# Kernel optimization log

Hardware: AMD Instinct MI355X
Metric: run time of the kernel (lower is better)

## Reference

```python
import jax, jax.numpy as jnp
import numpy as np

NEG_SLOPE = 0.2

def setup_inputs() -> dict:
    key = jax.random.key(0)
    k1, k2, k3, k4 = jax.random.split(key, 4)
    N, K, C_IN, C_OUT = 8192, 4, 512, 512
    inputs = jax.random.normal(k1, (N, C_IN), dtype=jnp.float32)
    adj_set = jax.random.uniform(k2, (K, N, N), dtype=jnp.float32)
    att = jax.random.uniform(k3, (K,), dtype=jnp.float32)
    # xavier_uniform for w
    limit = float(np.sqrt(6.0 / (C_IN + C_OUT)))
    w = jax.random.uniform(k4, (C_IN, C_OUT), minval=-limit, maxval=limit, dtype=jnp.float32)
    b = jnp.zeros((C_OUT,), dtype=jnp.float32)
    return {"inputs": inputs, "adj_set": adj_set, "att": att, "w": w, "b": b}

def reference(inputs, adj_set, att, w, b):
    # support: [N, C_out]
    support = inputs @ w + b
    # residual=True path: outputs = sum_i att[i] * (adj_i @ support)
    #                             = (sum_i att[i] * adj_i) @ support
    combined_adj = jnp.einsum('k,knm->nm', att, adj_set)  # [N, N]
    outputs = combined_adj @ support                       # [N, C_out]
    # LeakyReLU(negative_slope=0.2)
    return jnp.where(outputs >= 0, outputs, NEG_SLOPE * outputs)
```

## Files before the change

### kernel.cpp

```cpp
#include <hip/hip_runtime.h>

#define LP 40

typedef __attribute__((ext_vector_type(8))) short short8;
typedef __attribute__((ext_vector_type(4))) short short4t;
typedef __attribute__((ext_vector_type(4))) float f32x4;

__device__ __forceinline__ short f2bf(float f) {
  unsigned u = __builtin_bit_cast(unsigned, f);
  u += 0x7FFFu + ((u >> 16) & 1u);
  return (short)(u >> 16);
}

__device__ __forceinline__ float lrelu(float v) { return v >= 0.f ? v : 0.2f * v; }

__global__ __launch_bounds__(256) void k_wt(const float* __restrict__ w,
                                            short* __restrict__ wt) {
  __shared__ float t[64][65];
  int c0 = (blockIdx.x & 7) * 64;
  int n0 = (blockIdx.x >> 3) * 64;
  int r  = threadIdx.x >> 4;
  int q4 = (threadIdx.x & 15) * 4;
  for (int i = 0; i < 4; i++) {
    int c = r + i * 16;
    f32x4 v = *(const f32x4*)(w + (size_t)(c0 + c) * 512 + (n0 + q4));
    t[c][q4 + 0] = v[0]; t[c][q4 + 1] = v[1]; t[c][q4 + 2] = v[2]; t[c][q4 + 3] = v[3];
  }
  __syncthreads();
  for (int i = 0; i < 4; i++) {
    int n = r + i * 16;
    short4t o;
    for (int j = 0; j < 4; j++) o[j] = f2bf(t[q4 + j][n]);
    *(short4t*)(wt + (size_t)(n0 + n) * 512 + (c0 + q4)) = o;
  }
}

__global__ __launch_bounds__(512, 2) void k_support(const float* __restrict__ inp,
                                                    const short* __restrict__ wt,
                                                    const float* __restrict__ bias,
                                                    short* __restrict__ sup) {
  __shared__ __align__(16) short As[512 * LP];
  __shared__ __align__(16) short Bs[64 * LP];
  const int tid = threadIdx.x;
  const int m0 = blockIdx.x * 64;
  const int wave = tid >> 6, lane = tid & 63;
  const int wn = wave >> 1, wm = wave & 1;
  const int lr = lane & 15, lk = lane >> 4;
  const int bm = tid >> 3, bk = (tid & 7) * 4;
  f32x4 acc[8][2] = {};
  short8 ar[4]; f32x4 br;
  auto loadA = [&](int s) {
    const short* p = wt + (size_t)tid * 512 + s * 32;
    ar[0] = *(const short8*)(p);      ar[1] = *(const short8*)(p + 8);
    ar[2] = *(const short8*)(p + 16); ar[3] = *(const short8*)(p + 24);
  };
  auto loadB = [&](int s) {
    br = *(const f32x4*)(inp + (size_t)(m0 + bm) * 512 + s * 32 + bk);
  };
  loadA(0); loadB(0);
  for (int s = 0; s < 16; s++) {
    short* ad = As + tid * LP;
    *(short8*)(ad) = ar[0]; *(short8*)(ad + 8) = ar[1];
    *(short8*)(ad + 16) = ar[2]; *(short8*)(ad + 24) = ar[3];
    short4t bo;
    for (int j = 0; j < 4; j++) bo[j] = f2bf(br[j]);
    *(short4t*)(Bs + bm * LP + bk) = bo;
    __syncthreads();
    if (s + 1 < 16) { loadA(s + 1); loadB(s + 1); }
    short8 af[8], bfr[2];
    for (int nf = 0; nf < 8; nf++)
      af[nf] = *(const short8*)(As + (wn * 128 + nf * 16 + lr) * LP + lk * 8);
    for (int mf = 0; mf < 2; mf++)
      bfr[mf] = *(const short8*)(Bs + (wm * 32 + mf * 16 + lr) * LP + lk * 8);
    for (int nf = 0; nf < 8; nf++)
      for (int mf = 0; mf < 2; mf++)
        acc[nf][mf] = __builtin_amdgcn_mfma_f32_16x16x32_bf16(af[nf], bfr[mf], acc[nf][mf], 0, 0, 0);
    __syncthreads();
  }
  for (int nf = 0; nf < 8; nf++) {
    int nb = wn * 128 + nf * 16 + lk * 4;
    for (int mf = 0; mf < 2; mf++) {
      int m = m0 + wm * 32 + mf * 16 + lr;
      for (int j = 0; j < 4; j++) {
        int n = nb + j;
        sup[(size_t)n * 8192 + m] = f2bf(acc[nf][mf][j] + bias[n]);
      }
    }
  }
}

__global__ __launch_bounds__(512, 2) void k_main(const float* __restrict__ adj,
                                                 const float* __restrict__ att,
                                                 const short* __restrict__ sup,
                                                 float* __restrict__ part,
                                                 float* __restrict__ outp,
                                                 int ksplit) {
  __shared__ __align__(16) short Bs[2][128 * LP];
  const int tid = threadIdx.x;
  const int b = blockIdx.x;
  const int xpk = 8 / ksplit;
  const int xcd = b & 7;
  const int kc = xcd / xpk;
  const int m0 = ((b >> 3) * xpk + (xcd % xpk)) * 128;
  const int kchunk = 8192 / ksplit;
  const int nsteps = kchunk / 32;
  const int kbase = kc * kchunk;
  const float t0 = att[0], t1 = att[1], t2 = att[2], t3 = att[3];
  const int wave = tid >> 6, lane = tid & 63;
  const int lr = lane & 15, lk = lane >> 4;
  const int srow = tid >> 2, koff = (tid & 3) * 8;
  f32x4 acc[4][8] = {};
  const float* adjp = adj + (size_t)(m0 + srow) * 8192 + kbase + koff;
  const short* supp = sup + (size_t)(wave * 64 + lr) * 8192 + kbase + lk * 8;
  f32x4 br[8];
  auto loadAdj = [&](int s) {
    const float* q = adjp + (size_t)s * 32;
#pragma unroll
    for (int mt = 0; mt < 4; mt++) {
      br[mt * 2]     = __builtin_nontemporal_load((const f32x4*)(q + ((size_t)mt << 26)));
      br[mt * 2 + 1] = __builtin_nontemporal_load((const f32x4*)(q + ((size_t)mt << 26) + 4));
    }
  };
  loadAdj(0);
  int p = 0;
  for (int s = 0; s < nsteps; s++) {
    short8 af[4];
#pragma unroll
    for (int nf = 0; nf < 4; nf++)
      af[nf] = *(const short8*)(supp + (size_t)(nf * 16) * 8192 + s * 32);
    short8 bo;
#pragma unroll
    for (int k2 = 0; k2 < 8; k2++) {
      int h = k2 >> 2, j = k2 & 3;
      float c = t0 * br[h][j] + t1 * br[2 + h][j] + t2 * br[4 + h][j] + t3 * br[6 + h][j];
      bo[k2] = f2bf(c);
    }
    *(short8*)(Bs[p] + srow * LP + koff) = bo;
    __syncthreads();
    if (s + 1 < nsteps) loadAdj(s + 1);
    short8 bfr[8];
#pragma unroll
    for (int mf = 0; mf < 8; mf++)
      bfr[mf] = *(const short8*)(Bs[p] + (mf * 16 + lr) * LP + lk * 8);
#pragma unroll
    for (int nf = 0; nf < 4; nf++)
#pragma unroll
      for (int mf = 0; mf < 8; mf++)
        acc[nf][mf] = __builtin_amdgcn_mfma_f32_16x16x32_bf16(af[nf], bfr[mf], acc[nf][mf], 0, 0, 0);
    p ^= 1;
  }
#pragma unroll
  for (int nf = 0; nf < 4; nf++) {
    int n = wave * 64 + nf * 16 + lk * 4;
#pragma unroll
    for (int mf = 0; mf < 8; mf++) {
      int m = m0 + mf * 16 + lr;
      f32x4 v = acc[nf][mf];
      if (ksplit == 1) {
        for (int j = 0; j < 4; j++) v[j] = lrelu(v[j]);
        __builtin_nontemporal_store(v, (f32x4*)(outp + (size_t)m * 512 + n));
      } else {
        __builtin_nontemporal_store(v, (f32x4*)(part + ((size_t)kc << 22) + (size_t)m * 512 + n));
      }
    }
  }
}

__global__ __launch_bounds__(256) void k_reduce(const float* __restrict__ part,
                                                float* __restrict__ outp, int ksplit) {
  const size_t total = (size_t)8192 * 512 / 4;
  for (size_t i = (size_t)blockIdx.x * 256 + threadIdx.x; i < total;
       i += (size_t)gridDim.x * 256) {
    f32x4 a = __builtin_nontemporal_load((const f32x4*)(part + i * 4));
    for (int k = 1; k < ksplit; k++) {
      f32x4 bv = __builtin_nontemporal_load((const f32x4*)(part + ((size_t)k << 22) + i * 4));
      for (int j = 0; j < 4; j++) a[j] += bv[j];
    }
    f32x4 v;
    for (int j = 0; j < 4; j++) v[j] = lrelu(a[j]);
    __builtin_nontemporal_store(v, (f32x4*)(outp + i * 4));
  }
}

extern "C" void kernel_launch(void* const* d_in, const int* in_sizes, int n_in,
                              void* d_out, int out_size, void* d_ws, size_t ws_size,
                              hipStream_t stream) {
  const float* inputs = (const float*)d_in[0];
  const float* adj    = (const float*)d_in[1];
  const float* att    = (const float*)d_in[2];
  const float* w      = (const float*)d_in[3];
  const float* bias   = (const float*)d_in[4];
  float* outp = (float*)d_out;

  char* ws = (char*)d_ws;
  short* sup  = (short*)(ws);
  short* wt   = (short*)(ws + (8u << 20));
  float* part = (float*)(ws + (9u << 20));

  const size_t base = (9ull << 20), psz = (1ull << 24);
  int ksplit = 1;
  if (ws_size >= base + 4 * psz) ksplit = 4;
  else if (ws_size >= base + 2 * psz) ksplit = 2;

  k_wt<<<64, 256, 0, stream>>>(w, wt);
  k_support<<<128, 512, 0, stream>>>(inputs, wt, bias, sup);
  k_main<<<64 * ksplit, 512, 0, stream>>>(adj, att, sup, part, outp, ksplit);
  if (ksplit > 1) k_reduce<<<1024, 256, 0, stream>>>(part, outp, ksplit);
}
```

Measured before the change: 337.3 us.

## Stream adjacency one matrix at a time over 128-wide K tiles in k_main

The main kernel's K step grows from 32 to 128. The adjacency loads are restructured so each thread streams one of the four adjacency matrices at a time through a two-slot register buffer, accumulating the weighted sum while the next matrix's load is in flight. This cuts barrier count per K and gives longer contiguous per-row reads, but enlarges the LDS tile (padded stride 136) and register pressure, which may reduce occupancy.

```diff
diff --git a/kernel.cpp b/kernel.cpp
--- a/kernel.cpp
+++ b/kernel.cpp
@@ -1,6 +1,7 @@
 #include <hip/hip_runtime.h>
 
-#define LP 40
+#define LP  40
+#define LPS 136
 
 typedef __attribute__((ext_vector_type(8))) short short8;
 typedef __attribute__((ext_vector_type(4))) short short4t;
@@ -95,7 +96,7 @@
                                                  float* __restrict__ part,
                                                  float* __restrict__ outp,
                                                  int ksplit) {
-  __shared__ __align__(16) short Bs[2][128 * LP];
+  __shared__ __align__(16) short Bs[2][128 * LPS];
   const int tid = threadIdx.x;
   const int b = blockIdx.x;
   const int xpk = 8 / ksplit;
@@ -103,50 +104,62 @@
   const int kc = xcd / xpk;
   const int m0 = ((b >> 3) * xpk + (xcd % xpk)) * 128;
   const int kchunk = 8192 / ksplit;
-  const int nsteps = kchunk / 32;
+  const int nbig = kchunk / 128;
   const int kbase = kc * kchunk;
   const float t0 = att[0], t1 = att[1], t2 = att[2], t3 = att[3];
   const int wave = tid >> 6, lane = tid & 63;
   const int lr = lane & 15, lk = lane >> 4;
-  const int srow = tid >> 2, koff = (tid & 3) * 8;
+  const int r = tid >> 2, q = tid & 3;
   f32x4 acc[4][8] = {};
-  const float* adjp = adj + (size_t)(m0 + srow) * 8192 + kbase + koff;
+  const float* abase = adj + (size_t)(m0 + r) * 8192 + kbase + q * 4;
   const short* supp = sup + (size_t)(wave * 64 + lr) * 8192 + kbase + lk * 8;
-  f32x4 br[8];
-  auto loadAdj = [&](int s) {
-    const float* q = adjp + (size_t)s * 32;
-#pragma unroll
-    for (int mt = 0; mt < 4; mt++) {
-      br[mt * 2]     = __builtin_nontemporal_load((const f32x4*)(q + ((size_t)mt << 26)));
-      br[mt * 2 + 1] = __builtin_nontemporal_load((const f32x4*)(q + ((size_t)mt << 26) + 4));
-    }
+
+  f32x4 R[2][8];
+  auto loadMat = [&](int slot, int mat, int s) {
+    const float* p = abase + ((size_t)mat << 26) + s * 128;
+#pragma unroll
+    for (int j = 0; j < 8; j++)
+      R[slot][j] = __builtin_nontemporal_load((const f32x4*)(p + j * 16));
   };
-  loadAdj(0);
+  loadMat(0, 0, 0);
   int p = 0;
-  for (int s = 0; s < nsteps; s++) {
-    short8 af[4];
-#pragma unroll
-    for (int nf = 0; nf < 4; nf++)
-      af[nf] = *(const short8*)(supp + (size_t)(nf * 16) * 8192 + s * 32);
-    short8 bo;
-#pragma unroll
-    for (int k2 = 0; k2 < 8; k2++) {
-      int h = k2 >> 2, j = k2 & 3;
-      float c = t0 * br[h][j] + t1 * br[2 + h][j] + t2 * br[4 + h][j] + t3 * br[6 + h][j];
-      bo[k2] = f2bf(c);
-    }
-    *(short8*)(Bs[p] + srow * LP + koff) = bo;
+  for (int s = 0; s < nbig; s++) {
+    f32x4 par[8];
+    loadMat(1, 1, s);
+#pragma unroll
+    for (int j = 0; j < 8; j++) { f32x4 v = R[0][j]; for (int e = 0; e < 4; e++) par[j][e] = t0 * v[e]; }
+    loadMat(0, 2, s);
+#pragma unroll
+    for (int j = 0; j < 8; j++) { f32x4 v = R[1][j]; for (int e = 0; e < 4; e++) par[j][e] += t1 * v[e]; }
+    loadMat(1, 3, s);
+#pragma unroll
+    for (int j = 0; j < 8; j++) { f32x4 v = R[0][j]; for (int e = 0; e < 4; e++) par[j][e] += t2 * v[e]; }
+    if (s + 1 < nbig) loadMat(0, 0, s + 1);
+#pragma unroll
+    for (int j = 0; j < 8; j++) { f32x4 v = R[1][j]; for (int e = 0; e < 4; e++) par[j][e] += t3 * v[e]; }
+    short* brow = Bs[p] + r * LPS + q * 4;
+#pragma unroll
+    for (int j = 0; j < 8; j++) {
+      short4t o;
+      for (int e = 0; e < 4; e++) o[e] = f2bf(par[j][e]);
+      *(short4t*)(brow + j * 16) = o;
+    }
     __syncthreads();
-    if (s + 1 < nsteps) loadAdj(s + 1);
-    short8 bfr[8];
-#pragma unroll
-    for (int mf = 0; mf < 8; mf++)
-      bfr[mf] = *(const short8*)(Bs[p] + (mf * 16 + lr) * LP + lk * 8);
-#pragma unroll
-    for (int nf = 0; nf < 4; nf++)
+#pragma unroll
+    for (int sub = 0; sub < 4; sub++) {
+      short8 af[4], bfr[8];
+#pragma unroll
+      for (int nf = 0; nf < 4; nf++)
+        af[nf] = *(const short8*)(supp + (size_t)(nf * 16) * 8192 + s * 128 + sub * 32);
 #pragma unroll
       for (int mf = 0; mf < 8; mf++)
-        acc[nf][mf] = __builtin_amdgcn_mfma_f32_16x16x32_bf16(af[nf], bfr[mf], acc[nf][mf], 0, 0, 0);
+        bfr[mf] = *(const short8*)(Bs[p] + (mf * 16 + lr) * LPS + sub * 32 + lk * 8);
+#pragma unroll
+      for (int nf = 0; nf < 4; nf++)
+#pragma unroll
+        for (int mf = 0; mf < 8; mf++)
+          acc[nf][mf] = __builtin_amdgcn_mfma_f32_16x16x32_bf16(af[nf], bfr[mf], acc[nf][mf], 0, 0, 0);
+    }
     p ^= 1;
   }
 #pragma unroll
```

After: 356.4 us. +5.7%, slower.

## Deepen adjacency prefetch to three steps with smaller M tiles and ksplit 2

Applied to the files above, without the earlier changes.

Halves the k_main M tile from 128 to 64 rows so each thread loads one float4 per adjacency slice, and doubles the block count. Adjacency loads are now issued three k-steps ahead through a four-slot register ring in a manually unrolled loop, to keep more HBM requests in flight on this bandwidth-bound stream. The K split drops from 4 to 2, which shrinks the partial-sum buffer and the reduce traffic. In exchange, the support operand is re-read from memory by twice as many row tiles, and the register ring adds register pressure.

```diff
diff --git a/kernel.cpp b/kernel.cpp
--- a/kernel.cpp
+++ b/kernel.cpp
@@ -1,6 +1,7 @@
 #include <hip/hip_runtime.h>
 
-#define LP 40
+#define LP  40
+#define LPB 40
 
 typedef __attribute__((ext_vector_type(8))) short short8;
 typedef __attribute__((ext_vector_type(4))) short short4t;
@@ -89,71 +90,72 @@
   }
 }
 
+#define ISSUE(SL, S) {                                                          \
+    const float* p_ = abase + (size_t)(S) * 32;                                 \
+    R[SL][0] = __builtin_nontemporal_load((const f32x4*)(p_));                  \
+    R[SL][1] = __builtin_nontemporal_load((const f32x4*)(p_ + (1ull << 26)));   \
+    R[SL][2] = __builtin_nontemporal_load((const f32x4*)(p_ + (2ull << 26)));   \
+    R[SL][3] = __builtin_nontemporal_load((const f32x4*)(p_ + (3ull << 26)));   \
+  }
+
+#define STEP(U) {                                                               \
+    const int s_ = s0 + (U);                                                    \
+    if (s_ + 3 < nsteps) ISSUE(((U) + 3) & 3, s_ + 3);                          \
+    short8 af[4];                                                               \
+    _Pragma("unroll") for (int nf = 0; nf < 4; nf++)                            \
+      af[nf] = *(const short8*)(supp + (size_t)(nf * 16) * 8192 + (size_t)s_ * 32); \
+    f32x4 c;                                                                    \
+    _Pragma("unroll") for (int e = 0; e < 4; e++)                               \
+      c[e] = t0 * R[(U)][0][e] + t1 * R[(U)][1][e]                              \
+           + t2 * R[(U)][2][e] + t3 * R[(U)][3][e];                             \
+    short4t o;                                                                  \
+    _Pragma("unroll") for (int e = 0; e < 4; e++) o[e] = f2bf(c[e]);            \
+    *(short4t*)(Bs[(U) & 1] + r * LPB + q * 4) = o;                             \
+    __syncthreads();                                                            \
+    short8 bfr[4];                                                              \
+    _Pragma("unroll") for (int mf = 0; mf < 4; mf++)                            \
+      bfr[mf] = *(const short8*)(Bs[(U) & 1] + (mf * 16 + lr) * LPB + lk * 8);  \
+    _Pragma("unroll") for (int nf = 0; nf < 4; nf++)                            \
+      _Pragma("unroll") for (int mf = 0; mf < 4; mf++)                          \
+        acc[nf][mf] = __builtin_amdgcn_mfma_f32_16x16x32_bf16(af[nf], bfr[mf],  \
+                                                              acc[nf][mf], 0, 0, 0); \
+  }
+
 __global__ __launch_bounds__(512, 2) void k_main(const float* __restrict__ adj,
                                                  const float* __restrict__ att,
                                                  const short* __restrict__ sup,
                                                  float* __restrict__ part,
                                                  float* __restrict__ outp,
                                                  int ksplit) {
-  __shared__ __align__(16) short Bs[2][128 * LP];
+  __shared__ __align__(16) short Bs[2][64 * LPB];
   const int tid = threadIdx.x;
   const int b = blockIdx.x;
   const int xpk = 8 / ksplit;
   const int xcd = b & 7;
   const int kc = xcd / xpk;
-  const int m0 = ((b >> 3) * xpk + (xcd % xpk)) * 128;
+  const int m0 = ((b >> 3) * xpk + (xcd % xpk)) * 64;
   const int kchunk = 8192 / ksplit;
   const int nsteps = kchunk / 32;
   const int kbase = kc * kchunk;
   const float t0 = att[0], t1 = att[1], t2 = att[2], t3 = att[3];
   const int wave = tid >> 6, lane = tid & 63;
   const int lr = lane & 15, lk = lane >> 4;
-  const int srow = tid >> 2, koff = (tid & 3) * 8;
-  f32x4 acc[4][8] = {};
-  const float* adjp = adj + (size_t)(m0 + srow) * 8192 + kbase + koff;
+  const int r = tid >> 3, q = tid & 7;
+  f32x4 acc[4][4] = {};
+  const float* abase = adj + (size_t)(m0 + r) * 8192 + kbase + q * 4;
   const short* supp = sup + (size_t)(wave * 64 + lr) * 8192 + kbase + lk * 8;
-  f32x4 br[8];
-  auto loadAdj = [&](int s) {
-    const float* q = adjp + (size_t)s * 32;
-#pragma unroll
-    for (int mt = 0; mt < 4; mt++) {
-      br[mt * 2]     = __builtin_nontemporal_load((const f32x4*)(q + ((size_t)mt << 26)));
-      br[mt * 2 + 1] = __builtin_nontemporal_load((const f32x4*)(q + ((size_t)mt << 26) + 4));
-    }
-  };
-  loadAdj(0);
-  int p = 0;
-  for (int s = 0; s < nsteps; s++) {
-    short8 af[4];
-#pragma unroll
-    for (int nf = 0; nf < 4; nf++)
-      af[nf] = *(const short8*)(supp + (size_t)(nf * 16) * 8192 + s * 32);
-    short8 bo;
-#pragma unroll
-    for (int k2 = 0; k2 < 8; k2++) {
-      int h = k2 >> 2, j = k2 & 3;
-      float c = t0 * br[h][j] + t1 * br[2 + h][j] + t2 * br[4 + h][j] + t3 * br[6 + h][j];
-      bo[k2] = f2bf(c);
-    }
-    *(short8*)(Bs[p] + srow * LP + koff) = bo;
-    __syncthreads();
-    if (s + 1 < nsteps) loadAdj(s + 1);
-    short8 bfr[8];
-#pragma unroll
-    for (int mf = 0; mf < 8; mf++)
-      bfr[mf] = *(const short8*)(Bs[p] + (mf * 16 + lr) * LP + lk * 8);
-#pragma unroll
-    for (int nf = 0; nf < 4; nf++)
-#pragma unroll
-      for (int mf = 0; mf < 8; mf++)
-        acc[nf][mf] = __builtin_amdgcn_mfma_f32_16x16x32_bf16(af[nf], bfr[mf], acc[nf][mf], 0, 0, 0);
-    p ^= 1;
-  }
+  f32x4 R[4][4];
+
+  ISSUE(0, 0); ISSUE(1, 1); ISSUE(2, 2);
+  for (int s0 = 0; s0 < nsteps; s0 += 4) {
+    STEP(0) STEP(1) STEP(2) STEP(3)
+  }
+
 #pragma unroll
   for (int nf = 0; nf < 4; nf++) {
     int n = wave * 64 + nf * 16 + lk * 4;
 #pragma unroll
-    for (int mf = 0; mf < 8; mf++) {
+    for (int mf = 0; mf < 4; mf++) {
       int m = m0 + mf * 16 + lr;
       f32x4 v = acc[nf][mf];
       if (ksplit == 1) {
@@ -198,12 +200,10 @@
   float* part = (float*)(ws + (9u << 20));
 
   const size_t base = (9ull << 20), psz = (1ull << 24);
-  int ksplit = 1;
-  if (ws_size >= base + 4 * psz) ksplit = 4;
-  else if (ws_size >= base + 2 * psz) ksplit = 2;
+  int ksplit = (ws_size >= base + 2 * psz) ? 2 : 1;
 
   k_wt<<<64, 256, 0, stream>>>(w, wt);
   k_support<<<128, 512, 0, stream>>>(inputs, wt, bias, sup);
-  k_main<<<64 * ksplit, 512, 0, stream>>>(adj, att, sup, part, outp, ksplit);
+  k_main<<<128 * ksplit, 512, 0, stream>>>(adj, att, sup, part, outp, ksplit);
   if (ksplit > 1) k_reduce<<<1024, 256, 0, stream>>>(part, outp, ksplit);
 }
```

Result: faster. 317.7 us (-5.8%).

## Stream adjacency tiles into LDS via global_load_lds with 1024-thread blocks

Applied to the files above, without the earlier changes.

The main kernel now loads adjacency tiles straight from global memory into a double-buffered LDS staging area with global_load_lds, instead of through registers. It then combines the four attention-weighted matrices from LDS into bf16. The block grows to 1024 threads (16 waves) with a 2x8 wave tiling, which halves the per-wave accumulators, and synchronisation uses explicit waitcnt, sched_barrier and s_barrier. This is meant to raise the number of memory requests in flight and hide HBM latency on the bandwidth-bound adjacency stream. In exchange it uses about 136KB of LDS per block, and the hand-written waitcnt and wrap-around prefetch bring correctness and scheduling risk.

```diff
diff --git a/kernel.cpp b/kernel.cpp
--- a/kernel.cpp
+++ b/kernel.cpp
@@ -1,6 +1,7 @@
 #include <hip/hip_runtime.h>
 
-#define LP 40
+#define LP  40
+#define LPB 40
 
 typedef __attribute__((ext_vector_type(8))) short short8;
 typedef __attribute__((ext_vector_type(4))) short short4t;
@@ -89,13 +90,14 @@
   }
 }
 
-__global__ __launch_bounds__(512, 2) void k_main(const float* __restrict__ adj,
-                                                 const float* __restrict__ att,
-                                                 const short* __restrict__ sup,
-                                                 float* __restrict__ part,
-                                                 float* __restrict__ outp,
-                                                 int ksplit) {
-  __shared__ __align__(16) short Bs[2][128 * LP];
+__global__ __launch_bounds__(1024, 4) void k_main(const float* __restrict__ adj,
+                                                  const float* __restrict__ att,
+                                                  const short* __restrict__ sup,
+                                                  float* __restrict__ part,
+                                                  float* __restrict__ outp,
+                                                  int ksplit) {
+  __shared__ __align__(16) float rawA[2][4 * 128 * 32];
+  __shared__ __align__(16) short Bs[2][128 * LPB];
   const int tid = threadIdx.x;
   const int b = blockIdx.x;
   const int xpk = 8 / ksplit;
@@ -106,55 +108,81 @@
   const int nsteps = kchunk / 32;
   const int kbase = kc * kchunk;
   const float t0 = att[0], t1 = att[1], t2 = att[2], t3 = att[3];
-  const int wave = tid >> 6, lane = tid & 63;
-  const int lr = lane & 15, lk = lane >> 4;
-  const int srow = tid >> 2, koff = (tid & 3) * 8;
-  f32x4 acc[4][8] = {};
-  const float* adjp = adj + (size_t)(m0 + srow) * 8192 + kbase + koff;
-  const short* supp = sup + (size_t)(wave * 64 + lr) * 8192 + kbase + lk * 8;
-  f32x4 br[8];
-  auto loadAdj = [&](int s) {
-    const float* q = adjp + (size_t)s * 32;
-#pragma unroll
-    for (int mt = 0; mt < 4; mt++) {
-      br[mt * 2]     = __builtin_nontemporal_load((const f32x4*)(q + ((size_t)mt << 26)));
-      br[mt * 2 + 1] = __builtin_nontemporal_load((const f32x4*)(q + ((size_t)mt << 26) + 4));
-    }
+  const int w = tid >> 6, l = tid & 63;
+  const int lr = l & 15, lk = l >> 4;
+  const int n0w = (w >> 1) * 64;
+  const int mw = (w & 1) * 64;
+  const int crow = tid >> 3, coct = tid & 7;
+  f32x4 acc[4][4] = {};
+  const short* supbase = sup + (size_t)(n0w + lr) * 8192 + kbase + lk * 8;
+
+  size_t gofs[4];
+  int ldso[4];
+#pragma unroll
+  for (int i = 0; i < 4; i++) {
+    int c = w * 4 + i;
+    int mat = c >> 4, r0 = (c & 15) * 8;
+    gofs[i] = ((size_t)mat << 26) + (size_t)(m0 + r0 + (l >> 3)) * 8192 + kbase + (l & 7) * 4;
+    ldso[i] = c * 1024;
+  }
+  auto gl = [&](int i, int ss, int pp) {
+    const float* g = adj + gofs[i] + (size_t)ss * 32;
+    char* d = (char*)rawA[pp] + ldso[i];
+    __builtin_amdgcn_global_load_lds(
+        (const __attribute__((address_space(1))) unsigned*)g,
+        (__attribute__((address_space(3))) unsigned*)d, 16, 0, 0);
   };
-  loadAdj(0);
+
+#pragma unroll
+  for (int i = 0; i < 4; i++) gl(i, 0, 0);
+
   int p = 0;
   for (int s = 0; s < nsteps; s++) {
     short8 af[4];
 #pragma unroll
     for (int nf = 0; nf < 4; nf++)
-      af[nf] = *(const short8*)(supp + (size_t)(nf * 16) * 8192 + s * 32);
-    short8 bo;
-#pragma unroll
-    for (int k2 = 0; k2 < 8; k2++) {
-      int h = k2 >> 2, j = k2 & 3;
-      float c = t0 * br[h][j] + t1 * br[2 + h][j] + t2 * br[4 + h][j] + t3 * br[6 + h][j];
-      bo[k2] = f2bf(c);
-    }
-    *(short8*)(Bs[p] + srow * LP + koff) = bo;
-    __syncthreads();
-    if (s + 1 < nsteps) loadAdj(s + 1);
-    short8 bfr[8];
-#pragma unroll
-    for (int mf = 0; mf < 8; mf++)
-      bfr[mf] = *(const short8*)(Bs[p] + (mf * 16 + lr) * LP + lk * 8);
+      af[nf] = *(const short8*)(supbase + (size_t)(nf * 16) * 8192 + s * 32);
+    __builtin_amdgcn_sched_barrier(0);
+    int sn = (s + 1) & (nsteps - 1);
+#pragma unroll
+    for (int i = 0; i < 4; i++) gl(i, sn, p ^ 1);
+    __builtin_amdgcn_sched_barrier(0);
+    asm volatile("s_waitcnt vmcnt(8)" ::: "memory");
+    __builtin_amdgcn_sched_barrier(0);
+    __builtin_amdgcn_s_barrier();
+    {
+      const float* rb = rawA[p] + crow * 32 + coct * 4;
+      f32x4 v0 = *(const f32x4*)(rb);
+      f32x4 v1 = *(const f32x4*)(rb + 4096);
+      f32x4 v2 = *(const f32x4*)(rb + 8192);
+      f32x4 v3 = *(const f32x4*)(rb + 12288);
+      short4t o;
+#pragma unroll
+      for (int e = 0; e < 4; e++)
+        o[e] = f2bf(t0 * v0[e] + t1 * v1[e] + t2 * v2[e] + t3 * v3[e]);
+      *(short4t*)(Bs[p] + crow * LPB + coct * 4) = o;
+    }
+    asm volatile("s_waitcnt lgkmcnt(0)" ::: "memory");
+    __builtin_amdgcn_sched_barrier(0);
+    __builtin_amdgcn_s_barrier();
+    short8 bfr[4];
+#pragma unroll
+    for (int mf = 0; mf < 4; mf++)
+      bfr[mf] = *(const short8*)(Bs[p] + (mw + mf * 16 + lr) * LPB + lk * 8);
 #pragma unroll
     for (int nf = 0; nf < 4; nf++)
 #pragma unroll
-      for (int mf = 0; mf < 8; mf++)
+      for (int mf = 0; mf < 4; mf++)
         acc[nf][mf] = __builtin_amdgcn_mfma_f32_16x16x32_bf16(af[nf], bfr[mf], acc[nf][mf], 0, 0, 0);
     p ^= 1;
   }
+
 #pragma unroll
   for (int nf = 0; nf < 4; nf++) {
-    int n = wave * 64 + nf * 16 + lk * 4;
-#pragma unroll
-    for (int mf = 0; mf < 8; mf++) {
-      int m = m0 + mf * 16 + lr;
+    int n = n0w + nf * 16 + lk * 4;
+#pragma unroll
+    for (int mf = 0; mf < 4; mf++) {
+      int m = m0 + mw + mf * 16 + lr;
       f32x4 v = acc[nf][mf];
       if (ksplit == 1) {
         for (int j = 0; j < 4; j++) v[j] = lrelu(v[j]);
@@ -204,6 +232,6 @@
 
   k_wt<<<64, 256, 0, stream>>>(w, wt);
   k_support<<<128, 512, 0, stream>>>(inputs, wt, bias, sup);
-  k_main<<<64 * ksplit, 512, 0, stream>>>(adj, att, sup, part, outp, ksplit);
+  k_main<<<64 * ksplit, 1024, 0, stream>>>(adj, att, sup, part, outp, ksplit);
   if (ksplit > 1) k_reduce<<<1024, 256, 0, stream>>>(part, outp, ksplit);
 }
```

After: 334.9 us. Within noise of the previous version (-0.7%).
